# Performance work log

Measured on AMD Instinct MI355X. Metric: run time of the kernel, lower is better.

The kernel has to match this reference:

```python
import jax, jax.numpy as jnp
import numpy as np

# static config (matches init_kwargs)
B, CIN, L = 32, 128, 4096
COUT, K = 256, 5
PAD_SIZE = 2
INPUT_SCALE = 0.05
OUTPUT_SCALE = 0.1
INPUT_ZP = -3
OUTPUT_ZP = -128
QMIN, QMAX = -128, 127  # 8-bit signed range


def setup_inputs() -> dict:
    key = jax.random.key(0)
    k1, k2, k3, k4 = jax.random.split(key, 4)
    x = jax.random.normal(k1, (B, CIN, L), dtype=jnp.float32)
    weight = jax.random.randint(k2, (COUT, CIN, K), -127, 128, dtype=jnp.int32).astype(jnp.int8)
    # shifted quantized bias (int32), plausible magnitude
    bias = jax.random.randint(k3, (COUT,), -20000, 20000, dtype=jnp.int32)
    # per-output-channel weight scale
    weight_scale = jax.random.uniform(k4, (COUT,), dtype=jnp.float32, minval=1e-3, maxval=1e-2)
    return {"x": x, "weight": weight, "bias": bias, "weight_scale": weight_scale}


def reference(x, weight, bias, weight_scale):
    # --- linear_quantize (first_layer) ---
    xq = jnp.round(x / INPUT_SCALE) + INPUT_ZP
    xq = jnp.clip(xq, QMIN, QMAX).astype(jnp.int8)
    # --- ReplicationPad1d(pad_size) ---
    xq = jnp.pad(xq, ((0, 0), (0, 0), (PAD_SIZE, PAD_SIZE)), mode="edge")
    # --- int8 conv1d with int32 accumulation ---
    acc = jax.lax.conv_general_dilated(
        xq.astype(jnp.int32), weight.astype(jnp.int32),
        window_strides=(1,), padding=[(0, 0)],
        dimension_numbers=("NCH", "OIH", "NCH"))  # [B, COUT, Lout]
    acc = acc + bias[None, :, None]
    # --- per-channel requantization ---
    scale = (INPUT_SCALE * weight_scale / OUTPUT_SCALE)[None, :, None]
    out = acc.astype(jnp.float32) * scale + OUTPUT_ZP
    out = jnp.clip(jnp.round(out), QMIN, QMAX).astype(jnp.int8)
    return out
```

## Files before the change

kernel.cpp:

```cpp
#include <hip/hip_runtime.h>


#define B_    32
#define CIN   128
#define LEN   4096
#define COUT  256
#define KW    5
#define TROWS 136

#define WTF_BYTES (KW * 2 * 16 * 64 * 16)

typedef int            i32x4 __attribute__((ext_vector_type(4)));
typedef signed char    s8;

__device__ __forceinline__ s8 quant_i8(float xv) {
    float q = rintf(xv * 20.0f) - 3.0f;
    q = fminf(fmaxf(q, -128.0f), 127.0f);
    return (s8)(int)q;
}

__global__ __launch_bounds__(256) void wprep_kernel(
        const int* __restrict__ w, const int* __restrict__ bias,
        const float* __restrict__ wscale,
        s8* __restrict__ wtf, float* __restrict__ tbl)
{
    int o    = blockIdx.x * 256 + threadIdx.x;
    int lane = o & 63, frag = o >> 6;
    int k    = frag >> 5;
    int s    = (frag >> 4) & 1;
    int co   = ((frag & 15) << 4) + (lane & 15);
    int ci   = (s << 6) + ((lane >> 4) << 4);
    union { s8 c[16]; i32x4 v; } q;
    #pragma unroll
    for (int j = 0; j < 16; ++j)
        q.c[j] = (s8)w[co * (CIN * KW) + (ci + j) * KW + k];
    *(i32x4*)(wtf + (size_t)frag * 1024 + lane * 16) = q.v;

    if (blockIdx.x == 0) {
        int c = threadIdx.x;
        float sc = __fdiv_rn(__fmul_rn(0.05f, wscale[c]), 0.1f);
        tbl[c]       = sc;
        tbl[256 + c] = fmaf((float)bias[c], sc, -128.0f);
    }
}

__global__ __launch_bounds__(256, 4) void conv_fused(
        const float* __restrict__ x, const s8* __restrict__ wtf,
        const float* __restrict__ tbl, int* __restrict__ out)
{
    __shared__ __align__(16) s8 smem[TROWS * CIN];

    int orig  = (blockIdx.x & 7) * 256 + (blockIdx.x >> 3);
    int ch    = orig & 1;
    int ltile = (orig >> 1) & 31;
    int b     = orig >> 6;
    int l0    = ltile << 7;
    int tid   = threadIdx.x;
    int wid   = tid >> 6, lane = tid & 63;
    int lr    = lane & 15, lh = lane >> 4;
    int cog   = (ch << 7) + ((wid & 1) << 6);
    int wl    = (wid >> 1) << 6;

    const float* xb = x + (size_t)b * CIN * LEN;

    for (int p = wid; p < 24; p += 4) {
        int row = ((p >> 3) << 6) + lane;
        int c   = p & 7;
        if (row < TROWS) {
            int gl = l0 - 4 + row;
            gl = min(max(gl, 0), LEN - 1);
            const float* src = xb + (size_t)(c << 4) * LEN + gl;
            union { s8 cc[16]; i32x4 v; } q;
            #pragma unroll
            for (int j = 0; j < 16; ++j)
                q.cc[j] = quant_i8(src[(size_t)j * LEN]);
            *(i32x4*)(smem + (row << 7) + ((c ^ (row & 7)) << 4)) = q.v;
        }
    }
    __syncthreads();

    i32x4 acc[4][4] = {};
    #pragma unroll
    for (int k = 0; k < KW; ++k) {
        #pragma unroll
        for (int s = 0; s < 2; ++s) {
            i32x4 af[4];
            #pragma unroll
            for (int ct = 0; ct < 4; ++ct)
                af[ct] = *(const i32x4*)(
                    wtf + (size_t)((k << 5) + (s << 4) + (cog >> 4) + ct) * 1024 + lane * 16);
            i32x4 bf[4];
            int chunk = (s << 2) + lh;
            #pragma unroll
            for (int lt = 0; lt < 4; ++lt) {
                int row = wl + (lt << 4) + lr + k + 2;
                bf[lt] = *(const i32x4*)(smem + (row << 7) + ((chunk ^ (row & 7)) << 4));
            }
            #pragma unroll
            for (int ct = 0; ct < 4; ++ct)
                #pragma unroll
                for (int lt = 0; lt < 4; ++lt)
                    acc[ct][lt] = __builtin_amdgcn_mfma_i32_16x16x64_i8(
                        bf[lt], af[ct], acc[ct][lt], 0, 0, 0);
        }
    }

    size_t outb = (size_t)b * COUT * LEN;
    #pragma unroll
    for (int ct = 0; ct < 4; ++ct) {
        int co = cog + (ct << 4) + lr;
        float scv = tbl[co];
        float off = tbl[256 + co];
        int* orow = out + outb + (size_t)co * LEN + l0 + wl + (lh << 2);
        #pragma unroll
        for (int lt = 0; lt < 4; ++lt) {
            i32x4 pk;
            #pragma unroll
            for (int r = 0; r < 4; ++r) {
                float o = rintf(fmaf((float)acc[ct][lt][r], scv, off));
                o = fminf(fmaxf(o, -128.0f), 127.0f);
                pk[r] = (int)o;
            }
            *(i32x4*)(orow + (lt << 4)) = pk;
        }
    }
}

extern "C" void kernel_launch(void* const* d_in, const int* in_sizes, int n_in,
                              void* d_out, int out_size, void* d_ws, size_t ws_size,
                              hipStream_t stream)
{
    const float* x    = (const float*)d_in[0];
    const int*   w    = (const int*)d_in[1];
    const int*   bias = (const int*)d_in[2];
    const float* wsc  = (const float*)d_in[3];
    int* out = (int*)d_out;

    s8*    wtf = (s8*)d_ws;
    float* tbl = (float*)((char*)d_ws + WTF_BYTES);

    wprep_kernel<<<dim3(40), dim3(256), 0, stream>>>(w, bias, wsc, wtf, tbl);
    conv_fused<<<dim3(2048), dim3(256), 0, stream>>>(x, wtf, tbl, out);
}
```

Measured before the change: 59.65 us.

## Pre-quantize input into padded swizzled int8 buffer and stage via direct LDS loads

Input quantization and edge replication move out of the conv kernel into the prep kernel. The prep kernel writes a padded, row-swizzled int8 copy of x to workspace using vectorized float4 reads. The conv kernel then fills shared memory with global_load_lds straight from that buffer, which removes repeated float loads and quantization from the halo overlap. The cost is an extra global write and read of the int8 tensor (about 16.8 MB) plus a dependency on a larger workspace.

Result: slower. 62.26 us (+4.4%).

```diff
diff --git a/kernel.cpp b/kernel.cpp
--- a/kernel.cpp
+++ b/kernel.cpp
@@ -6,12 +6,16 @@
 #define LEN   4096
 #define COUT  256
 #define KW    5
+#define RPAD  4104
 #define TROWS 136
 
+#define XQS_BYTES ((size_t)B_ * RPAD * CIN)
 #define WTF_BYTES (KW * 2 * 16 * 64 * 16)
 
-typedef int            i32x4 __attribute__((ext_vector_type(4)));
-typedef signed char    s8;
+typedef int          i32x4 __attribute__((ext_vector_type(4)));
+typedef float        f32x4 __attribute__((ext_vector_type(4)));
+typedef signed char  s8;
+typedef unsigned int u32;
 
 __device__ __forceinline__ s8 quant_i8(float xv) {
     float q = rintf(xv * 20.0f) - 3.0f;
@@ -19,33 +23,72 @@
     return (s8)(int)q;
 }
 
-__global__ __launch_bounds__(256) void wprep_kernel(
-        const int* __restrict__ w, const int* __restrict__ bias,
-        const float* __restrict__ wscale,
-        s8* __restrict__ wtf, float* __restrict__ tbl)
+__global__ __launch_bounds__(256) void prep_kernel(
+        const float* __restrict__ x, const int* __restrict__ w,
+        const int* __restrict__ bias, const float* __restrict__ wscale,
+        s8* __restrict__ xqs, s8* __restrict__ wtf, float* __restrict__ tbl)
 {
-    int o    = blockIdx.x * 256 + threadIdx.x;
-    int lane = o & 63, frag = o >> 6;
-    int k    = frag >> 5;
-    int s    = (frag >> 4) & 1;
-    int co   = ((frag & 15) << 4) + (lane & 15);
-    int ci   = (s << 6) + ((lane >> 4) << 4);
-    union { s8 c[16]; i32x4 v; } q;
-    #pragma unroll
-    for (int j = 0; j < 16; ++j)
-        q.c[j] = (s8)w[co * (CIN * KW) + (ci + j) * KW + k];
-    *(i32x4*)(wtf + (size_t)frag * 1024 + lane * 16) = q.v;
+    int bx = blockIdx.x, tid = threadIdx.x;
+    if (bx < 544) {
+        int b = bx / 17, rg = bx % 17;
+        int lane = tid & 63, wv = tid >> 6;
+        int rq = rg * 64 + lane;
+        if (rq >= 1026) return;
+        int r0 = rq << 2;
+        const float* xbb = x + (size_t)b * CIN * LEN;
+        bool interior = (rq >= 1) && (rq <= 1024);
+        #pragma unroll
+        for (int it = 0; it < 2; ++it) {
+            int c = wv + (it << 2);
+            union { s8 cc[16]; i32x4 v; } q[4];
+            if (interior) {
+                const float* src = xbb + (size_t)(c << 4) * LEN + (r0 - 4);
+                #pragma unroll
+                for (int j = 0; j < 16; ++j) {
+                    f32x4 f = *(const f32x4*)(src + (size_t)j * LEN);
+                    #pragma unroll
+                    for (int m = 0; m < 4; ++m) q[m].cc[j] = quant_i8(f[m]);
+                }
+            } else {
+                #pragma unroll
+                for (int j = 0; j < 16; ++j)
+                    #pragma unroll
+                    for (int m = 0; m < 4; ++m) {
+                        int gl = r0 + m - 4;
+                        gl = min(max(gl, 0), LEN - 1);
+                        q[m].cc[j] = quant_i8(xbb[(size_t)((c << 4) + j) * LEN + gl]);
+                    }
+            }
+            #pragma unroll
+            for (int m = 0; m < 4; ++m) {
+                int r = r0 + m;
+                *(i32x4*)(xqs + ((size_t)b * RPAD + r) * CIN + ((c ^ (r & 7)) << 4)) = q[m].v;
+            }
+        }
+    } else {
+        int o    = (bx - 544) * 256 + tid;
+        int lane = o & 63, frag = o >> 6;
+        int k    = frag >> 5;
+        int s    = (frag >> 4) & 1;
+        int co   = ((frag & 15) << 4) + (lane & 15);
+        int ci   = (s << 6) + ((lane >> 4) << 4);
+        union { s8 c[16]; i32x4 v; } q;
+        #pragma unroll
+        for (int j = 0; j < 16; ++j)
+            q.c[j] = (s8)w[co * (CIN * KW) + (ci + j) * KW + k];
+        *(i32x4*)(wtf + (size_t)frag * 1024 + lane * 16) = q.v;
 
-    if (blockIdx.x == 0) {
-        int c = threadIdx.x;
-        float sc = __fdiv_rn(__fmul_rn(0.05f, wscale[c]), 0.1f);
-        tbl[c]       = sc;
-        tbl[256 + c] = fmaf((float)bias[c], sc, -128.0f);
+        if (bx == 544) {
+            int c = tid;
+            float sc = __fdiv_rn(__fmul_rn(0.05f, wscale[c]), 0.1f);
+            tbl[c]       = sc;
+            tbl[256 + c] = fmaf((float)bias[c], sc, -128.0f);
+        }
     }
 }
 
 __global__ __launch_bounds__(256, 4) void conv_fused(
-        const float* __restrict__ x, const s8* __restrict__ wtf,
+        const s8* __restrict__ xqs, const s8* __restrict__ wtf,
         const float* __restrict__ tbl, int* __restrict__ out)
 {
     __shared__ __align__(16) s8 smem[TROWS * CIN];
@@ -61,22 +104,12 @@
     int cog   = (ch << 7) + ((wid & 1) << 6);
     int wl    = (wid >> 1) << 6;
 
-    const float* xb = x + (size_t)b * CIN * LEN;
-
-    for (int p = wid; p < 24; p += 4) {
-        int row = ((p >> 3) << 6) + lane;
-        int c   = p & 7;
-        if (row < TROWS) {
-            int gl = l0 - 4 + row;
-            gl = min(max(gl, 0), LEN - 1);
-            const float* src = xb + (size_t)(c << 4) * LEN + gl;
-            union { s8 cc[16]; i32x4 v; } q;
-            #pragma unroll
-            for (int j = 0; j < 16; ++j)
-                q.cc[j] = quant_i8(src[(size_t)j * LEN]);
-            *(i32x4*)(smem + (row << 7) + ((c ^ (row & 7)) << 4)) = q.v;
-        }
-    }
+    const s8* src = xqs + ((size_t)b * RPAD + l0) * CIN;
+    for (int i = wid; i < 17; i += 4)
+        __builtin_amdgcn_global_load_lds(
+            (const __attribute__((address_space(1))) u32*)(src + (i << 10) + (lane << 4)),
+            (__attribute__((address_space(3))) u32*)(smem + (i << 10)),
+            16, 0, 0);
     __syncthreads();
 
     i32x4 acc[4][4] = {};
@@ -136,9 +169,10 @@
     const float* wsc  = (const float*)d_in[3];
     int* out = (int*)d_out;
 
-    s8*    wtf = (s8*)d_ws;
-    float* tbl = (float*)((char*)d_ws + WTF_BYTES);
+    s8*    xqs = (s8*)d_ws;
+    s8*    wtf = xqs + XQS_BYTES;
+    float* tbl = (float*)(wtf + WTF_BYTES);
 
-    wprep_kernel<<<dim3(40), dim3(256), 0, stream>>>(w, bias, wsc, wtf, tbl);
-    conv_fused<<<dim3(2048), dim3(256), 0, stream>>>(x, wtf, tbl, out);
+    prep_kernel<<<dim3(584), dim3(256), 0, stream>>>(x, w, bias, wsc, xqs, wtf, tbl);
+    conv_fused<<<dim3(2048), dim3(256), 0, stream>>>(xqs, wtf, tbl, out);
 }
```
